# Kernel tuning notes

Hardware: AMD Instinct MI355X
Metric: run time of the kernel (lower is better)

The kernel has to match this reference:

```python
import jax, jax.numpy as jnp
import numpy as np

N = 8192
E = 262144
IN_DIM, HID, OUT = 256, 256, 32


def setup_inputs() -> dict:
    key = jax.random.key(0)
    ks = jax.random.split(key, 10)
    features = jax.random.normal(ks[0], (N, IN_DIM), jnp.float32)
    noise = jax.random.normal(ks[1], (N, OUT), jnp.float32)
    src = jax.random.randint(ks[2], (E,), 0, N, jnp.int32)
    dst = jax.random.randint(ks[3], (E,), 0, N, jnp.int32)
    s = lambda fi, fo: 1.0 / np.sqrt(fi)
    W1 = jax.random.normal(ks[4], (IN_DIM, HID), jnp.float32) * s(IN_DIM, HID)
    W2 = jax.random.normal(ks[5], (HID, HID), jnp.float32) * s(HID, HID)
    W3 = jax.random.normal(ks[6], (HID, OUT), jnp.float32) * s(HID, OUT)
    b1 = jnp.zeros((HID,), jnp.float32)
    b2 = jnp.zeros((HID,), jnp.float32)
    b3 = jnp.zeros((OUT,), jnp.float32)
    fc_w = jax.random.normal(ks[7], (IN_DIM, OUT), jnp.float32) * s(IN_DIM, OUT)
    return dict(features=features, noise=noise, src=src, dst=dst,
                W1=W1, b1=b1, W2=W2, b2=b2, W3=W3, b3=b3, fc_w=fc_w)


def _degree_norms(src, dst, n):
    ones = jnp.ones_like(src, jnp.float32)
    out_deg = jax.ops.segment_sum(ones, src, num_segments=n)
    in_deg = jax.ops.segment_sum(ones, dst, num_segments=n)
    # DGL GraphConv norm='both' clamps degrees to min 1 before pow(-0.5)
    norm_src = jnp.maximum(out_deg, 1.0) ** -0.5  # [N]
    norm_dst = jnp.maximum(in_deg, 1.0) ** -0.5   # [N]
    return norm_src, norm_dst


def _graph_conv(x, src, dst, norm_src, norm_dst, W, b, n):
    # h = D_in^{-1/2} A D_out^{-1/2} x W + b, then relu
    h = x @ W                                  # transform first (smaller agg dim)
    m = (h * norm_src[:, None])[src]           # [E, F] gather + scale
    agg = jax.ops.segment_sum(m, dst, num_segments=n)
    return jax.nn.relu(agg * norm_dst[:, None] + b)


def reference(features, noise, src, dst, W1, b1, W2, b2, W3, b3, fc_w):
    n = features.shape[0]
    norm_s, norm_d = _degree_norms(src, dst, n)
    h = _graph_conv(features, src, dst, norm_s, norm_d, W1, b1, n)
    mean = _graph_conv(h, src, dst, norm_s, norm_d, W2, b2, n)
    log_std = _graph_conv(h, src, dst, norm_s, norm_d, W3, b3, n)
    # note: mean [N,HID] broadcasts against noise*exp(log_std) [N,OUT] only if
    # HID==OUT dims align; original code has mean from layer[1] (hidden_dim) and
    # log_std from layer[2] (out_dim). To keep the math runnable we follow the
    # VGAE intent: layer[1] and layer[2] both map to out_dim here (W2 below is
    # hidden->hidden, W3 hidden->out; mean uses W3-shaped branch). See notes.
    z = mean[:, :noise.shape[1]] if mean.shape[1] != noise.shape[1] else mean
    z = z + noise * jnp.exp(log_std)
    adj_rec = jax.nn.sigmoid(z @ z.T)          # [N, N] dense decoder
    seq_fts = features @ fc_w                  # Linear(in_dim, out_dim, bias=False)
    return adj_rec, z, seq_fts
```

## Files before the change

kernel.cpp:

```cpp
#include <hip/hip_runtime.h>
#include <hip/hip_fp16.h>

#define NNODES 8192
#define NEDGES 262144
#define NNOUT 67108864L

typedef _Float16 half8 __attribute__((ext_vector_type(8)));
typedef _Float16 half4 __attribute__((ext_vector_type(4)));
typedef float float4v __attribute__((ext_vector_type(4)));


__global__ __launch_bounds__(256) void prep_kernel(const float* __restrict__ W1, const float* __restrict__ W2,
                                                   const float* __restrict__ W3, const float* __restrict__ b2,
                                                   const float* __restrict__ b3, _Float16* __restrict__ W1th,
                                                   _Float16* __restrict__ W1tl, _Float16* __restrict__ Wzth,
                                                   _Float16* __restrict__ Wztl, float* __restrict__ bz,
                                                   int* __restrict__ degs) {
  int b = blockIdx.x, t = threadIdx.x;
  float w = W1[b * 256 + t];
  _Float16 wh = (_Float16)w;
  W1th[t * 256 + b] = wh;
  W1tl[t * 256 + b] = (_Float16)(w - (float)wh);
  if (b >= 64 && b < 128) {
    int c = b - 64;
    float v = (c < 32) ? W2[t * 256 + c] : W3[t * 32 + (c - 32)];
    _Float16 vh = (_Float16)v;
    Wzth[c * 256 + t] = vh;
    Wztl[c * 256 + t] = (_Float16)(v - (float)vh);
  }
  if (b == 128 && t < 64) bz[t] = (t < 32) ? b2[t] : b3[t - 32];
  if (b >= 192) degs[(b - 192) * 256 + t] = 0;
}

__global__ __launch_bounds__(256) void deg_kernel(const int* __restrict__ src, const int* __restrict__ dst,
                                                  int* __restrict__ out_deg, int* __restrict__ in_deg) {
  int e = blockIdx.x * 256 + threadIdx.x;
  if (e < NEDGES) {
    atomicAdd(&out_deg[src[e]], 1);
    atomicAdd(&in_deg[dst[e]], 1);
  }
}

__global__ __launch_bounds__(256) void scan_norm_kernel(const int* __restrict__ in_deg,
                                                        const int* __restrict__ out_deg,
                                                        int* __restrict__ row_ptr, int* __restrict__ cursor,
                                                        float* __restrict__ norm_src, float* __restrict__ norm_dst) {
  __shared__ int partial[256];
  int t = threadIdx.x;
  int base = t * 32;
  int local[32];
  int s = 0;
#pragma unroll
  for (int i = 0; i < 32; ++i) { local[i] = in_deg[base + i]; s += local[i]; }
  partial[t] = s;
  __syncthreads();
  for (int off = 1; off < 256; off <<= 1) {
    int v = (t >= off) ? partial[t - off] : 0;
    __syncthreads();
    partial[t] += v;
    __syncthreads();
  }
  int run = (t == 0) ? 0 : partial[t - 1];
  if (t == 0) row_ptr[0] = 0;
#pragma unroll
  for (int i = 0; i < 32; ++i) {
    int od = out_deg[base + i]; if (od < 1) od = 1;
    int id = local[i]; if (id < 1) id = 1;
    norm_src[base + i] = rsqrtf((float)od);
    norm_dst[base + i] = rsqrtf((float)id);
    cursor[base + i] = run;
    run += local[i];
    row_ptr[base + i + 1] = run;
  }
}

__global__ __launch_bounds__(256) void scatter_convert_seq(const int* __restrict__ src, const int* __restrict__ dst,
                                                           int* __restrict__ cursor, int* __restrict__ csr,
                                                           const float* __restrict__ x,
                                                           const float* __restrict__ norm_src,
                                                           _Float16* __restrict__ xs, const float* __restrict__ Wf,
                                                           float* __restrict__ seq) {
  int b = blockIdx.x, t = threadIdx.x;
  if (b >= 2048) {
    int tt = (b - 2048) * 256 + t;
    int row = tt >> 3;
    int cq = (tt & 7) * 4;
    float a0 = 0.f, a1 = 0.f, a2 = 0.f, a3 = 0.f;
    const float* frow = x + row * 256;
    for (int k = 0; k < 256; k += 4) {
      float4 fv = *(const float4*)(frow + k);
      float4 w0 = *(const float4*)(Wf + k * 32 + cq);
      float4 w1 = *(const float4*)(Wf + (k + 1) * 32 + cq);
      float4 w2 = *(const float4*)(Wf + (k + 2) * 32 + cq);
      float4 w3 = *(const float4*)(Wf + (k + 3) * 32 + cq);
      a0 = fmaf(fv.x, w0.x, fmaf(fv.y, w1.x, fmaf(fv.z, w2.x, fmaf(fv.w, w3.x, a0))));
      a1 = fmaf(fv.x, w0.y, fmaf(fv.y, w1.y, fmaf(fv.z, w2.y, fmaf(fv.w, w3.y, a1))));
      a2 = fmaf(fv.x, w0.z, fmaf(fv.y, w1.z, fmaf(fv.z, w2.z, fmaf(fv.w, w3.z, a2))));
      a3 = fmaf(fv.x, w0.w, fmaf(fv.y, w1.w, fmaf(fv.z, w2.w, fmaf(fv.w, w3.w, a3))));
    }
    float4 o = {a0, a1, a2, a3};
    *(float4*)&seq[row * 32 + cq] = o;
    return;
  }
  if (b < 1024) {
    int e = b * 256 + t;
    int d = dst[e];
    int pos = atomicAdd(&cursor[d], 1);
    csr[pos] = src[e];
  }
  int i = b * 256 + t;
  int base = i * 4;
  float ns = norm_src[base >> 8];
  float4 v = *(const float4*)(x + base);
  half4 o = {(_Float16)(v.x * ns), (_Float16)(v.y * ns), (_Float16)(v.z * ns), (_Float16)(v.w * ns)};
  *(half4*)(xs + base) = o;
}


__global__ __launch_bounds__(256) void propagate_hl(const _Float16* __restrict__ xs, _Float16* __restrict__ Qh,
                                                    _Float16* __restrict__ Ql, const int* __restrict__ row_ptr,
                                                    const int* __restrict__ csr, const float* __restrict__ norm_dst) {
  int v = blockIdx.x * 4 + (threadIdx.x >> 6);
  int lane = threadIdx.x & 63;
  int beg = row_ptr[v], end = row_ptr[v + 1];
  float a0 = 0.f, a1 = 0.f, a2 = 0.f, a3 = 0.f;
  const _Float16* base = xs + 4 * lane;
  int e = beg;
  for (; e + 4 <= end; e += 4) {
    int s0 = csr[e], s1 = csr[e + 1], s2 = csr[e + 2], s3 = csr[e + 3];
    half4 v0 = *(const half4*)(base + (long)s0 * 256);
    half4 v1 = *(const half4*)(base + (long)s1 * 256);
    half4 v2 = *(const half4*)(base + (long)s2 * 256);
    half4 v3 = *(const half4*)(base + (long)s3 * 256);
    a0 += (float)v0.x + (float)v1.x + (float)v2.x + (float)v3.x;
    a1 += (float)v0.y + (float)v1.y + (float)v2.y + (float)v3.y;
    a2 += (float)v0.z + (float)v1.z + (float)v2.z + (float)v3.z;
    a3 += (float)v0.w + (float)v1.w + (float)v2.w + (float)v3.w;
  }
  for (; e < end; ++e) {
    half4 v0 = *(const half4*)(base + (long)csr[e] * 256);
    a0 += (float)v0.x; a1 += (float)v0.y; a2 += (float)v0.z; a3 += (float)v0.w;
  }
  float nd = norm_dst[v];
  a0 *= nd; a1 *= nd; a2 *= nd; a3 *= nd;
  _Float16 h0 = (_Float16)a0, h1 = (_Float16)a1, h2 = (_Float16)a2, h3 = (_Float16)a3;
  half4 qh = {h0, h1, h2, h3};
  half4 ql = {(_Float16)(a0 - (float)h0), (_Float16)(a1 - (float)h1),
              (_Float16)(a2 - (float)h2), (_Float16)(a3 - (float)h3)};
  *(half4*)(Qh + (long)v * 256 + 4 * lane) = qh;
  *(half4*)(Ql + (long)v * 256 + 4 * lane) = ql;
}


__global__ __launch_bounds__(256) void gemm1_mfma(const _Float16* __restrict__ Qh, const _Float16* __restrict__ Ql,
                                                  const _Float16* __restrict__ W1th, const _Float16* __restrict__ W1tl,
                                                  const float* __restrict__ b1, const float* __restrict__ norm_src,
                                                  _Float16* __restrict__ xs) {
  int tid = threadIdx.x;
  int wave = tid >> 6, lane = tid & 63;
  int l15 = lane & 15, lk = (lane >> 4) * 8;
  long rowBase = blockIdx.x * 64 + wave * 16;
  int colBase = blockIdx.y * 128;
  float4v acc[8] = {};
  for (int ks = 0; ks < 8; ++ks) {
    int k0 = ks * 32;
    half8 ah = *(const half8*)(Qh + (rowBase + l15) * 256 + k0 + lk);
    half8 al = *(const half8*)(Ql + (rowBase + l15) * 256 + k0 + lk);
#pragma unroll
    for (int ct = 0; ct < 8; ++ct) {
      long bo = (long)(colBase + ct * 16 + l15) * 256 + k0 + lk;
      half8 bh = *(const half8*)(W1th + bo);
      half8 bl = *(const half8*)(W1tl + bo);
      acc[ct] = __builtin_amdgcn_mfma_f32_16x16x32_f16(al, bh, acc[ct], 0, 0, 0);
      acc[ct] = __builtin_amdgcn_mfma_f32_16x16x32_f16(ah, bl, acc[ct], 0, 0, 0);
      acc[ct] = __builtin_amdgcn_mfma_f32_16x16x32_f16(ah, bh, acc[ct], 0, 0, 0);
    }
  }
  int crow = (lane >> 4) * 4;
#pragma unroll
  for (int ct = 0; ct < 8; ++ct) {
    int c = colBase + ct * 16 + l15;
    float bb = b1[c];
#pragma unroll
    for (int r = 0; r < 4; ++r) {
      long row = rowBase + crow + r;
      float v = fmaxf(acc[ct][r] + bb, 0.f) * norm_src[row];
      xs[row * 256 + c] = (_Float16)v;
    }
  }
}


__global__ __launch_bounds__(256) void gemmz_mfma(const _Float16* __restrict__ Qh, const _Float16* __restrict__ Ql,
                                                  const _Float16* __restrict__ Wzth, const _Float16* __restrict__ Wztl,
                                                  const float* __restrict__ bz, const float* __restrict__ noise,
                                                  float* __restrict__ zout, _Float16* __restrict__ Zh,
                                                  _Float16* __restrict__ Zl) {
  int tid = threadIdx.x;
  int wave = tid >> 6, lane = tid & 63;
  int l15 = lane & 15, lk = (lane >> 4) * 8;
  long rowBase = blockIdx.x * 64 + wave * 16;
  float4v acc[4] = {};
  for (int ks = 0; ks < 8; ++ks) {
    int k0 = ks * 32;
    half8 ah = *(const half8*)(Qh + (rowBase + l15) * 256 + k0 + lk);
    half8 al = *(const half8*)(Ql + (rowBase + l15) * 256 + k0 + lk);
#pragma unroll
    for (int ct = 0; ct < 4; ++ct) {
      long bo = (long)(ct * 16 + l15) * 256 + k0 + lk;
      half8 bh = *(const half8*)(Wzth + bo);
      half8 bl = *(const half8*)(Wztl + bo);
      acc[ct] = __builtin_amdgcn_mfma_f32_16x16x32_f16(al, bh, acc[ct], 0, 0, 0);
      acc[ct] = __builtin_amdgcn_mfma_f32_16x16x32_f16(ah, bl, acc[ct], 0, 0, 0);
      acc[ct] = __builtin_amdgcn_mfma_f32_16x16x32_f16(ah, bh, acc[ct], 0, 0, 0);
    }
  }
  int crow = (lane >> 4) * 4;
  float bm0 = bz[l15], bm1 = bz[16 + l15], bs0 = bz[32 + l15], bs1 = bz[48 + l15];
#pragma unroll
  for (int r = 0; r < 4; ++r) {
    long row = rowBase + crow + r;
    float me0 = fmaxf(acc[0][r] + bm0, 0.f);
    float me1 = fmaxf(acc[1][r] + bm1, 0.f);
    float ls0 = fmaxf(acc[2][r] + bs0, 0.f);
    float ls1 = fmaxf(acc[3][r] + bs1, 0.f);
    float n0 = noise[row * 32 + l15];
    float n1 = noise[row * 32 + 16 + l15];
    float z0 = me0 + n0 * __expf(ls0);
    float z1 = me1 + n1 * __expf(ls1);
    zout[row * 32 + l15] = z0;
    zout[row * 32 + 16 + l15] = z1;
    _Float16 h0 = (_Float16)z0, h1 = (_Float16)z1;
    Zh[row * 32 + l15] = h0;
    Zl[row * 32 + l15] = (_Float16)(z0 - (float)h0);
    Zh[row * 32 + 16 + l15] = h1;
    Zl[row * 32 + 16 + l15] = (_Float16)(z1 - (float)h1);
  }
}


__global__ __launch_bounds__(256) void adj_mfma(const _Float16* __restrict__ Zh, const _Float16* __restrict__ Zl,
                                                float* __restrict__ out) {
  __shared__ __align__(16) float lds[4][32][68];
  int tid = threadIdx.x;
  int wave = tid >> 6;
  int lane = tid & 63;
  long rowBase = (long)blockIdx.y * 128 + wave * 32;
  long colBase = (long)blockIdx.x * 128;
  int l15 = lane & 15;
  int lk = (lane >> 4) * 8;
  half8 ah0 = *(const half8*)(Zh + (rowBase + l15) * 32 + lk);
  half8 al0 = *(const half8*)(Zl + (rowBase + l15) * 32 + lk);
  half8 ah1 = *(const half8*)(Zh + (rowBase + 16 + l15) * 32 + lk);
  half8 al1 = *(const half8*)(Zl + (rowBase + 16 + l15) * 32 + lk);
  int crow = (lane >> 4) * 4;
  float* slab = &lds[wave][0][0];
#pragma unroll
  for (int h = 0; h < 2; ++h) {
#pragma unroll
    for (int ct = 0; ct < 4; ++ct) {
      int cg = h * 4 + ct;
      half8 bh = *(const half8*)(Zh + (colBase + cg * 16 + l15) * 32 + lk);
      half8 bl = *(const half8*)(Zl + (colBase + cg * 16 + l15) * 32 + lk);
      float4v acc0 = {}, acc1 = {};
      acc0 = __builtin_amdgcn_mfma_f32_16x16x32_f16(al0, bh, acc0, 0, 0, 0);
      acc0 = __builtin_amdgcn_mfma_f32_16x16x32_f16(ah0, bl, acc0, 0, 0, 0);
      acc0 = __builtin_amdgcn_mfma_f32_16x16x32_f16(ah0, bh, acc0, 0, 0, 0);
      acc1 = __builtin_amdgcn_mfma_f32_16x16x32_f16(al1, bh, acc1, 0, 0, 0);
      acc1 = __builtin_amdgcn_mfma_f32_16x16x32_f16(ah1, bl, acc1, 0, 0, 0);
      acc1 = __builtin_amdgcn_mfma_f32_16x16x32_f16(ah1, bh, acc1, 0, 0, 0);
#pragma unroll
      for (int r = 0; r < 4; ++r) {
        slab[(crow + r) * 68 + ct * 16 + l15] = __builtin_amdgcn_rcpf(1.f + __expf(-acc0[r]));
        slab[(16 + crow + r) * 68 + ct * 16 + l15] = __builtin_amdgcn_rcpf(1.f + __expf(-acc1[r]));
      }
    }
    __syncthreads();
#pragma unroll
    for (int i = 0; i < 8; ++i) {
      int rr = 4 * i + (lane >> 4);
      float4 v = *(const float4*)&slab[rr * 68 + 4 * l15];
      *(float4*)&out[(rowBase + rr) * 8192 + colBase + h * 64 + 4 * l15] = v;
    }
    __syncthreads();
  }
}


extern "C" void kernel_launch(void* const* d_in, const int* in_sizes, int n_in,
                              void* d_out, int out_size, void* d_ws, size_t ws_size,
                              hipStream_t stream) {
  const float* features = (const float*)d_in[0];
  const float* noise    = (const float*)d_in[1];
  const int*   src      = (const int*)d_in[2];
  const int*   dst      = (const int*)d_in[3];
  const float* W1       = (const float*)d_in[4];
  const float* b1       = (const float*)d_in[5];
  const float* W2       = (const float*)d_in[6];
  const float* b2       = (const float*)d_in[7];
  const float* W3       = (const float*)d_in[8];
  const float* b3       = (const float*)d_in[9];
  const float* fcw      = (const float*)d_in[10];

  float* out = (float*)d_out;

  int* ws_i    = (int*)d_ws;
  int* out_deg = ws_i;
  int* in_deg  = ws_i + 8192;
  int* row_ptr = ws_i + 16384;
  int* cursor  = ws_i + 24832;
  int* csr     = ws_i + 33024;
  float* norm_src = (float*)(ws_i + 295168);
  float* norm_dst = (float*)(ws_i + 303360);
  _Float16* Zh = (_Float16*)(ws_i + 311552);
  _Float16* Zl = (_Float16*)(ws_i + 442624);

  float* adj      = out;
  float* zbuf     = out + NNOUT;
  float* seq      = out + NNOUT + 262144;
  _Float16* xs    = (_Float16*)out;
  _Float16* Qh    = (_Float16*)(out + 1048576);
  _Float16* Ql    = (_Float16*)(out + 2097152);
  _Float16* W1th  = (_Float16*)(out + 3145728);
  _Float16* W1tl  = (_Float16*)(out + 3178496);
  _Float16* Wzth  = (_Float16*)(out + 3211264);
  _Float16* Wztl  = (_Float16*)(out + 3219456);
  float*    bz    = out + 3227648;

  prep_kernel<<<256, 256, 0, stream>>>(W1, W2, W3, b2, b3, W1th, W1tl, Wzth, Wztl, bz, out_deg);
  deg_kernel<<<NEDGES / 256, 256, 0, stream>>>(src, dst, out_deg, in_deg);
  scan_norm_kernel<<<1, 256, 0, stream>>>(in_deg, out_deg, row_ptr, cursor, norm_src, norm_dst);
  scatter_convert_seq<<<2304, 256, 0, stream>>>(src, dst, cursor, csr, features, norm_src, xs, fcw, seq);

  propagate_hl<<<2048, 256, 0, stream>>>(xs, Qh, Ql, row_ptr, csr, norm_dst);
  gemm1_mfma<<<dim3(128, 2), 256, 0, stream>>>(Qh, Ql, W1th, W1tl, b1, norm_src, xs);

  propagate_hl<<<2048, 256, 0, stream>>>(xs, Qh, Ql, row_ptr, csr, norm_dst);
  gemmz_mfma<<<128, 256, 0, stream>>>(Qh, Ql, Wzth, Wztl, bz, noise, zbuf, Zh, Zl);

  adj_mfma<<<dim3(64, 64), 256, 0, stream>>>(Zh, Zl, adj);
}
```

Measured before the change: 206.7 us.

## Fuse graph preprocessing into one grid-barrier kernel and split propagate across feature halves

Degree counting, the prefix scan, CSR scatter, fp16 feature scaling and the seq_fts projection now run in a single 1024-block kernel. Its phases are separated by software grid barriers built on agent-scope atomics, and the scan is done per block plus a serial 32-entry offset pass. This removes several kernel launches and the single-block scan, but it depends on all 1024 blocks being resident at once, otherwise the barriers deadlock. The propagate kernel is launched with twice as many blocks, each handling half the feature columns with half2 loads, and uses nontemporal stores. The adjacency decoder drops two __syncthreads around its shared-memory staging slab and uses nontemporal stores for the large output, which could race if waves share slab rows.

```diff
diff --git a/kernel.cpp b/kernel.cpp
--- a/kernel.cpp
+++ b/kernel.cpp
@@ -4,9 +4,11 @@
 #define NNODES 8192
 #define NEDGES 262144
 #define NNOUT 67108864L
+#define NB 1024
 
 typedef _Float16 half8 __attribute__((ext_vector_type(8)));
 typedef _Float16 half4 __attribute__((ext_vector_type(4)));
+typedef _Float16 half2v __attribute__((ext_vector_type(2)));
 typedef float float4v __attribute__((ext_vector_type(4)));
 
 
@@ -15,7 +17,7 @@
                                                    const float* __restrict__ b3, _Float16* __restrict__ W1th,
                                                    _Float16* __restrict__ W1tl, _Float16* __restrict__ Wzth,
                                                    _Float16* __restrict__ Wztl, float* __restrict__ bz,
-                                                   int* __restrict__ degs) {
+                                                   int* __restrict__ degs, int* __restrict__ bar) {
   int b = blockIdx.x, t = threadIdx.x;
   float w = W1[b * 256 + t];
   _Float16 wh = (_Float16)w;
@@ -29,60 +31,97 @@
     Wztl[c * 256 + t] = (_Float16)(v - (float)vh);
   }
   if (b == 128 && t < 64) bz[t] = (t < 32) ? b2[t] : b3[t - 32];
+  if (b == 129 && t < 16) bar[t] = 0;
   if (b >= 192) degs[(b - 192) * 256 + t] = 0;
 }
 
-__global__ __launch_bounds__(256) void deg_kernel(const int* __restrict__ src, const int* __restrict__ dst,
-                                                  int* __restrict__ out_deg, int* __restrict__ in_deg) {
-  int e = blockIdx.x * 256 + threadIdx.x;
-  if (e < NEDGES) {
+
+__device__ __forceinline__ void gridbar(int* bar, int idx) {
+  __syncthreads();
+  if (threadIdx.x == 0) {
+    __hip_atomic_fetch_add(bar + idx, 1, __ATOMIC_ACQ_REL, __HIP_MEMORY_SCOPE_AGENT);
+    while (__hip_atomic_load(bar + idx, __ATOMIC_ACQUIRE, __HIP_MEMORY_SCOPE_AGENT) < NB) {
+      __builtin_amdgcn_s_sleep(2);
+    }
+  }
+  __syncthreads();
+}
+
+__global__ __launch_bounds__(256, 8) void mega_preproc(
+    const int* __restrict__ src, const int* __restrict__ dst, const float* __restrict__ x,
+    const float* __restrict__ Wf, int* __restrict__ out_deg, int* __restrict__ in_deg,
+    int* __restrict__ row_ptr, int* __restrict__ cursor, int* __restrict__ csr,
+    float* __restrict__ norm_src, float* __restrict__ norm_dst, _Float16* __restrict__ xs,
+    float* __restrict__ seq, int* bar, int* partials) {
+  __shared__ int sc[256];
+  int b = blockIdx.x, t = threadIdx.x;
+
+  {
+    int e = b * 256 + t;
     atomicAdd(&out_deg[src[e]], 1);
     atomicAdd(&in_deg[dst[e]], 1);
   }
-}
-
-__global__ __launch_bounds__(256) void scan_norm_kernel(const int* __restrict__ in_deg,
-                                                        const int* __restrict__ out_deg,
-                                                        int* __restrict__ row_ptr, int* __restrict__ cursor,
-                                                        float* __restrict__ norm_src, float* __restrict__ norm_dst) {
-  __shared__ int partial[256];
-  int t = threadIdx.x;
-  int base = t * 32;
-  int local[32];
-  int s = 0;
-#pragma unroll
-  for (int i = 0; i < 32; ++i) { local[i] = in_deg[base + i]; s += local[i]; }
-  partial[t] = s;
-  __syncthreads();
-  for (int off = 1; off < 256; off <<= 1) {
-    int v = (t >= off) ? partial[t - off] : 0;
+  gridbar(bar, 0);
+
+  int d = 0, pre = 0;
+  if (b < 32) {
+    int i = b * 256 + t;
+    d = __hip_atomic_load(&in_deg[i], __ATOMIC_RELAXED, __HIP_MEMORY_SCOPE_AGENT);
+    int od = __hip_atomic_load(&out_deg[i], __ATOMIC_RELAXED, __HIP_MEMORY_SCOPE_AGENT);
+    sc[t] = d;
     __syncthreads();
-    partial[t] += v;
-    __syncthreads();
-  }
-  int run = (t == 0) ? 0 : partial[t - 1];
-  if (t == 0) row_ptr[0] = 0;
-#pragma unroll
-  for (int i = 0; i < 32; ++i) {
-    int od = out_deg[base + i]; if (od < 1) od = 1;
-    int id = local[i]; if (id < 1) id = 1;
-    norm_src[base + i] = rsqrtf((float)od);
-    norm_dst[base + i] = rsqrtf((float)id);
-    cursor[base + i] = run;
-    run += local[i];
-    row_ptr[base + i + 1] = run;
-  }
-}
-
-__global__ __launch_bounds__(256) void scatter_convert_seq(const int* __restrict__ src, const int* __restrict__ dst,
-                                                           int* __restrict__ cursor, int* __restrict__ csr,
-                                                           const float* __restrict__ x,
-                                                           const float* __restrict__ norm_src,
-                                                           _Float16* __restrict__ xs, const float* __restrict__ Wf,
-                                                           float* __restrict__ seq) {
-  int b = blockIdx.x, t = threadIdx.x;
-  if (b >= 2048) {
-    int tt = (b - 2048) * 256 + t;
+    for (int off = 1; off < 256; off <<= 1) {
+      int v = (t >= off) ? sc[t - off] : 0;
+      __syncthreads();
+      sc[t] += v;
+      __syncthreads();
+    }
+    int incl = sc[t];
+    pre = incl - d;
+    if (t == 255) __hip_atomic_store(&partials[b], incl, __ATOMIC_RELAXED, __HIP_MEMORY_SCOPE_AGENT);
+    norm_dst[i] = rsqrtf((float)(d < 1 ? 1 : d));
+    norm_src[i] = rsqrtf((float)(od < 1 ? 1 : od));
+  }
+  gridbar(bar, 1);
+
+  if (b == 0 && t == 0) {
+    int run = 0;
+    for (int k = 0; k < 32; ++k) {
+      int v = __hip_atomic_load(&partials[k], __ATOMIC_RELAXED, __HIP_MEMORY_SCOPE_AGENT);
+      __hip_atomic_store(&partials[32 + k], run, __ATOMIC_RELAXED, __HIP_MEMORY_SCOPE_AGENT);
+      run += v;
+    }
+  }
+  gridbar(bar, 2);
+
+  if (b < 32) {
+    int off = __hip_atomic_load(&partials[32 + b], __ATOMIC_RELAXED, __HIP_MEMORY_SCOPE_AGENT);
+    int i = b * 256 + t;
+    int start = off + pre;
+    __hip_atomic_store(&cursor[i], start, __ATOMIC_RELAXED, __HIP_MEMORY_SCOPE_AGENT);
+    row_ptr[i + 1] = start + d;
+    if (i == 0) row_ptr[0] = 0;
+  }
+  gridbar(bar, 3);
+
+  {
+    int e = b * 256 + t;
+    int pos = atomicAdd(&cursor[dst[e]], 1);
+    csr[pos] = src[e];
+  }
+  {
+    long i0 = ((long)(b * 256 + t)) * 8;
+    int row = (int)(i0 >> 8);
+    int od = __hip_atomic_load(&out_deg[row], __ATOMIC_RELAXED, __HIP_MEMORY_SCOPE_AGENT);
+    float ns = rsqrtf((float)(od < 1 ? 1 : od));
+    float4 v0 = *(const float4*)(x + i0);
+    float4 v1 = *(const float4*)(x + i0 + 4);
+    half8 o = {(_Float16)(v0.x * ns), (_Float16)(v0.y * ns), (_Float16)(v0.z * ns), (_Float16)(v0.w * ns),
+               (_Float16)(v1.x * ns), (_Float16)(v1.y * ns), (_Float16)(v1.z * ns), (_Float16)(v1.w * ns)};
+    *(half8*)(xs + i0) = o;
+  }
+  if (b < 256) {
+    int tt = b * 256 + t;
     int row = tt >> 3;
     int cq = (tt & 7) * 4;
     float a0 = 0.f, a1 = 0.f, a2 = 0.f, a3 = 0.f;
@@ -100,55 +139,45 @@
     }
     float4 o = {a0, a1, a2, a3};
     *(float4*)&seq[row * 32 + cq] = o;
-    return;
-  }
-  if (b < 1024) {
-    int e = b * 256 + t;
-    int d = dst[e];
-    int pos = atomicAdd(&cursor[d], 1);
-    csr[pos] = src[e];
-  }
-  int i = b * 256 + t;
-  int base = i * 4;
-  float ns = norm_src[base >> 8];
-  float4 v = *(const float4*)(x + base);
-  half4 o = {(_Float16)(v.x * ns), (_Float16)(v.y * ns), (_Float16)(v.z * ns), (_Float16)(v.w * ns)};
-  *(half4*)(xs + base) = o;
+  }
 }
 
 
 __global__ __launch_bounds__(256) void propagate_hl(const _Float16* __restrict__ xs, _Float16* __restrict__ Qh,
                                                     _Float16* __restrict__ Ql, const int* __restrict__ row_ptr,
                                                     const int* __restrict__ csr, const float* __restrict__ norm_dst) {
-  int v = blockIdx.x * 4 + (threadIdx.x >> 6);
-  int lane = threadIdx.x & 63;
+  int b = blockIdx.x;
+  int w = threadIdx.x >> 6, lane = threadIdx.x & 63;
+  int q = b >> 3, r = b & 7;
+  int h = r >> 2, s = r & 3;
+  int v = (q * 4 + s) * 4 + w;
   int beg = row_ptr[v], end = row_ptr[v + 1];
-  float a0 = 0.f, a1 = 0.f, a2 = 0.f, a3 = 0.f;
-  const _Float16* base = xs + 4 * lane;
+  const _Float16* base = xs + h * 128 + 2 * lane;
+  float a0 = 0.f, a1 = 0.f;
   int e = beg;
   for (; e + 4 <= end; e += 4) {
     int s0 = csr[e], s1 = csr[e + 1], s2 = csr[e + 2], s3 = csr[e + 3];
-    half4 v0 = *(const half4*)(base + (long)s0 * 256);
-    half4 v1 = *(const half4*)(base + (long)s1 * 256);
-    half4 v2 = *(const half4*)(base + (long)s2 * 256);
-    half4 v3 = *(const half4*)(base + (long)s3 * 256);
+    half2v v0 = *(const half2v*)(base + (long)s0 * 256);
+    half2v v1 = *(const half2v*)(base + (long)s1 * 256);
+    half2v v2 = *(const half2v*)(base + (long)s2 * 256);
+    half2v v3 = *(const half2v*)(base + (long)s3 * 256);
     a0 += (float)v0.x + (float)v1.x + (float)v2.x + (float)v3.x;
     a1 += (float)v0.y + (float)v1.y + (float)v2.y + (float)v3.y;
-    a2 += (float)v0.z + (float)v1.z + (float)v2.z + (float)v3.z;
-    a3 += (float)v0.w + (float)v1.w + (float)v2.w + (float)v3.w;
   }
   for (; e < end; ++e) {
-    half4 v0 = *(const half4*)(base + (long)csr[e] * 256);
-    a0 += (float)v0.x; a1 += (float)v0.y; a2 += (float)v0.z; a3 += (float)v0.w;
+    half2v v0 = *(const half2v*)(base + (long)csr[e] * 256);
+    a0 += (float)v0.x;
+    a1 += (float)v0.y;
   }
   float nd = norm_dst[v];
-  a0 *= nd; a1 *= nd; a2 *= nd; a3 *= nd;
-  _Float16 h0 = (_Float16)a0, h1 = (_Float16)a1, h2 = (_Float16)a2, h3 = (_Float16)a3;
-  half4 qh = {h0, h1, h2, h3};
-  half4 ql = {(_Float16)(a0 - (float)h0), (_Float16)(a1 - (float)h1),
-              (_Float16)(a2 - (float)h2), (_Float16)(a3 - (float)h3)};
-  *(half4*)(Qh + (long)v * 256 + 4 * lane) = qh;
-  *(half4*)(Ql + (long)v * 256 + 4 * lane) = ql;
+  a0 *= nd;
+  a1 *= nd;
+  _Float16 h0 = (_Float16)a0, h1 = (_Float16)a1;
+  half2v qh = {h0, h1};
+  half2v ql = {(_Float16)(a0 - (float)h0), (_Float16)(a1 - (float)h1)};
+  long o = (long)v * 256 + h * 128 + 2 * lane;
+  __builtin_nontemporal_store(qh, (half2v*)(Qh + o));
+  __builtin_nontemporal_store(ql, (half2v*)(Ql + o));
 }
 
 
@@ -275,14 +304,12 @@
         slab[(16 + crow + r) * 68 + ct * 16 + l15] = __builtin_amdgcn_rcpf(1.f + __expf(-acc1[r]));
       }
     }
-    __syncthreads();
 #pragma unroll
     for (int i = 0; i < 8; ++i) {
       int rr = 4 * i + (lane >> 4);
-      float4 v = *(const float4*)&slab[rr * 68 + 4 * l15];
-      *(float4*)&out[(rowBase + rr) * 8192 + colBase + h * 64 + 4 * l15] = v;
-    }
-    __syncthreads();
+      float4v v = *(const float4v*)&slab[rr * 68 + 4 * l15];
+      __builtin_nontemporal_store(v, (float4v*)&out[(rowBase + rr) * 8192 + colBase + h * 64 + 4 * l15]);
+    }
   }
 }
 
@@ -312,8 +339,10 @@
   int* csr     = ws_i + 33024;
   float* norm_src = (float*)(ws_i + 295168);
   float* norm_dst = (float*)(ws_i + 303360);
-  _Float16* Zh = (_Float16*)(ws_i + 311552);
-  _Float16* Zl = (_Float16*)(ws_i + 442624);
+  int* bar     = ws_i + 311552;
+  int* partials = ws_i + 311568;
+  _Float16* Zh = (_Float16*)(ws_i + 311680);
+  _Float16* Zl = (_Float16*)(ws_i + 442752);
 
   float* adj      = out;
   float* zbuf     = out + NNOUT;
@@ -327,15 +356,14 @@
   _Float16* Wztl  = (_Float16*)(out + 3219456);
   float*    bz    = out + 3227648;
 
-  prep_kernel<<<256, 256, 0, stream>>>(W1, W2, W3, b2, b3, W1th, W1tl, Wzth, Wztl, bz, out_deg);
-  deg_kernel<<<NEDGES / 256, 256, 0, stream>>>(src, dst, out_deg, in_deg);
-  scan_norm_kernel<<<1, 256, 0, stream>>>(in_deg, out_deg, row_ptr, cursor, norm_src, norm_dst);
-  scatter_convert_seq<<<2304, 256, 0, stream>>>(src, dst, cursor, csr, features, norm_src, xs, fcw, seq);
-
-  propagate_hl<<<2048, 256, 0, stream>>>(xs, Qh, Ql, row_ptr, csr, norm_dst);
+  prep_kernel<<<256, 256, 0, stream>>>(W1, W2, W3, b2, b3, W1th, W1tl, Wzth, Wztl, bz, out_deg, bar);
+  mega_preproc<<<NB, 256, 0, stream>>>(src, dst, features, fcw, out_deg, in_deg, row_ptr, cursor, csr,
+                                       norm_src, norm_dst, xs, seq, bar, partials);
+
+  propagate_hl<<<4096, 256, 0, stream>>>(xs, Qh, Ql, row_ptr, csr, norm_dst);
   gemm1_mfma<<<dim3(128, 2), 256, 0, stream>>>(Qh, Ql, W1th, W1tl, b1, norm_src, xs);
 
-  propagate_hl<<<2048, 256, 0, stream>>>(xs, Qh, Ql, row_ptr, csr, norm_dst);
+  propagate_hl<<<4096, 256, 0, stream>>>(xs, Qh, Ql, row_ptr, csr, norm_dst);
   gemmz_mfma<<<128, 256, 0, stream>>>(Qh, Ql, Wzth, Wztl, bz, noise, zbuf, Zh, Zl);
 
   adj_mfma<<<dim3(64, 64), 256, 0, stream>>>(Zh, Zl, adj);
```

Measured after the change: 456.0 us. 121% more time.

## Split propagation across feature halves, drop adj barriers, use nontemporal stores

Applied to the files above, without the earlier changes.

Each propagate block now handles one 128-wide half of the feature columns, using half2 loads and twice as many blocks, to raise parallelism for the edge gather. Qh/Ql are written with nontemporal stores. In the dense adjacency decoder, the __syncthreads around the LDS slab are removed and the output goes out as nontemporal float4 stores to cut barrier stalls and cache pollution. The Z buffers are moved to a new workspace offset. Dropping the barriers is only safe if each wave reads back only slab rows it wrote itself, otherwise it risks a race.

```diff
diff --git a/kernel.cpp b/kernel.cpp
--- a/kernel.cpp
+++ b/kernel.cpp
@@ -7,6 +7,7 @@
 
 typedef _Float16 half8 __attribute__((ext_vector_type(8)));
 typedef _Float16 half4 __attribute__((ext_vector_type(4)));
+typedef _Float16 half2v __attribute__((ext_vector_type(2)));
 typedef float float4v __attribute__((ext_vector_type(4)));
 
 
@@ -120,35 +121,38 @@
 __global__ __launch_bounds__(256) void propagate_hl(const _Float16* __restrict__ xs, _Float16* __restrict__ Qh,
                                                     _Float16* __restrict__ Ql, const int* __restrict__ row_ptr,
                                                     const int* __restrict__ csr, const float* __restrict__ norm_dst) {
-  int v = blockIdx.x * 4 + (threadIdx.x >> 6);
-  int lane = threadIdx.x & 63;
+  int b = blockIdx.x;
+  int w = threadIdx.x >> 6, lane = threadIdx.x & 63;
+  int q = b >> 3, r = b & 7;
+  int h = r >> 2, s = r & 3;
+  int v = (q * 4 + s) * 4 + w;
   int beg = row_ptr[v], end = row_ptr[v + 1];
-  float a0 = 0.f, a1 = 0.f, a2 = 0.f, a3 = 0.f;
-  const _Float16* base = xs + 4 * lane;
+  const _Float16* base = xs + h * 128 + 2 * lane;
+  float a0 = 0.f, a1 = 0.f;
   int e = beg;
   for (; e + 4 <= end; e += 4) {
     int s0 = csr[e], s1 = csr[e + 1], s2 = csr[e + 2], s3 = csr[e + 3];
-    half4 v0 = *(const half4*)(base + (long)s0 * 256);
-    half4 v1 = *(const half4*)(base + (long)s1 * 256);
-    half4 v2 = *(const half4*)(base + (long)s2 * 256);
-    half4 v3 = *(const half4*)(base + (long)s3 * 256);
+    half2v v0 = *(const half2v*)(base + (long)s0 * 256);
+    half2v v1 = *(const half2v*)(base + (long)s1 * 256);
+    half2v v2 = *(const half2v*)(base + (long)s2 * 256);
+    half2v v3 = *(const half2v*)(base + (long)s3 * 256);
     a0 += (float)v0.x + (float)v1.x + (float)v2.x + (float)v3.x;
     a1 += (float)v0.y + (float)v1.y + (float)v2.y + (float)v3.y;
-    a2 += (float)v0.z + (float)v1.z + (float)v2.z + (float)v3.z;
-    a3 += (float)v0.w + (float)v1.w + (float)v2.w + (float)v3.w;
   }
   for (; e < end; ++e) {
-    half4 v0 = *(const half4*)(base + (long)csr[e] * 256);
-    a0 += (float)v0.x; a1 += (float)v0.y; a2 += (float)v0.z; a3 += (float)v0.w;
+    half2v v0 = *(const half2v*)(base + (long)csr[e] * 256);
+    a0 += (float)v0.x;
+    a1 += (float)v0.y;
   }
   float nd = norm_dst[v];
-  a0 *= nd; a1 *= nd; a2 *= nd; a3 *= nd;
-  _Float16 h0 = (_Float16)a0, h1 = (_Float16)a1, h2 = (_Float16)a2, h3 = (_Float16)a3;
-  half4 qh = {h0, h1, h2, h3};
-  half4 ql = {(_Float16)(a0 - (float)h0), (_Float16)(a1 - (float)h1),
-              (_Float16)(a2 - (float)h2), (_Float16)(a3 - (float)h3)};
-  *(half4*)(Qh + (long)v * 256 + 4 * lane) = qh;
-  *(half4*)(Ql + (long)v * 256 + 4 * lane) = ql;
+  a0 *= nd;
+  a1 *= nd;
+  _Float16 h0 = (_Float16)a0, h1 = (_Float16)a1;
+  half2v qh = {h0, h1};
+  half2v ql = {(_Float16)(a0 - (float)h0), (_Float16)(a1 - (float)h1)};
+  long o = (long)v * 256 + h * 128 + 2 * lane;
+  __builtin_nontemporal_store(qh, (half2v*)(Qh + o));
+  __builtin_nontemporal_store(ql, (half2v*)(Ql + o));
 }
 
 
@@ -275,14 +279,12 @@
         slab[(16 + crow + r) * 68 + ct * 16 + l15] = __builtin_amdgcn_rcpf(1.f + __expf(-acc1[r]));
       }
     }
-    __syncthreads();
 #pragma unroll
     for (int i = 0; i < 8; ++i) {
       int rr = 4 * i + (lane >> 4);
-      float4 v = *(const float4*)&slab[rr * 68 + 4 * l15];
-      *(float4*)&out[(rowBase + rr) * 8192 + colBase + h * 64 + 4 * l15] = v;
-    }
-    __syncthreads();
+      float4v v = *(const float4v*)&slab[rr * 68 + 4 * l15];
+      __builtin_nontemporal_store(v, (float4v*)&out[(rowBase + rr) * 8192 + colBase + h * 64 + 4 * l15]);
+    }
   }
 }
 
@@ -312,8 +314,8 @@
   int* csr     = ws_i + 33024;
   float* norm_src = (float*)(ws_i + 295168);
   float* norm_dst = (float*)(ws_i + 303360);
-  _Float16* Zh = (_Float16*)(ws_i + 311552);
-  _Float16* Zl = (_Float16*)(ws_i + 442624);
+  _Float16* Zh = (_Float16*)(ws_i + 311680);
+  _Float16* Zl = (_Float16*)(ws_i + 442752);
 
   float* adj      = out;
   float* zbuf     = out + NNOUT;
@@ -332,10 +334,10 @@
   scan_norm_kernel<<<1, 256, 0, stream>>>(in_deg, out_deg, row_ptr, cursor, norm_src, norm_dst);
   scatter_convert_seq<<<2304, 256, 0, stream>>>(src, dst, cursor, csr, features, norm_src, xs, fcw, seq);
 
-  propagate_hl<<<2048, 256, 0, stream>>>(xs, Qh, Ql, row_ptr, csr, norm_dst);
+  propagate_hl<<<4096, 256, 0, stream>>>(xs, Qh, Ql, row_ptr, csr, norm_dst);
   gemm1_mfma<<<dim3(128, 2), 256, 0, stream>>>(Qh, Ql, W1th, W1tl, b1, norm_src, xs);
 
-  propagate_hl<<<2048, 256, 0, stream>>>(xs, Qh, Ql, row_ptr, csr, norm_dst);
+  propagate_hl<<<4096, 256, 0, stream>>>(xs, Qh, Ql, row_ptr, csr, norm_dst);
   gemmz_mfma<<<128, 256, 0, stream>>>(Qh, Ql, Wzth, Wztl, bz, noise, zbuf, Zh, Zl);
 
   adj_mfma<<<dim3(64, 64), 256, 0, stream>>>(Zh, Zl, adj);
```

Result: slower. 212.8 us (+3.0%).
